# Performance work log

Hardware: AMD Instinct MI355X
Metric: run time of the kernel (lower is better)

## Reference

```python
import jax, jax.numpy as jnp
import numpy as np

DIM = 256
HEADS = 8
HEAD_DIM = DIM // HEADS
FFN = 1024
DIST_DECAY = 10.0
SCALING = HEAD_DIM ** -0.5
EPS = 1e-5


def _layer_norm(x, g, b):
    mu = jnp.mean(x, axis=-1, keepdims=True)
    var = jnp.mean((x - mu) ** 2, axis=-1, keepdims=True)
    return (x - mu) * jax.lax.rsqrt(var + EPS) * g + b


def setup_inputs() -> dict:
    key = jax.random.key(0)
    ks = jax.random.split(key, 20)
    B, N = 2, 192
    p = lambda k, shape: (jax.random.normal(k, shape, dtype=jnp.float32) * 0.02)
    return {
        "x": jax.random.normal(ks[0], (B, N, DIM), dtype=jnp.float32),
        "pos": jax.random.normal(ks[1], (B, N, 3), dtype=jnp.float32),
        "mask": jax.random.randint(ks[2], (B, N), 0, 2).astype(bool),
        "Wqkv": p(ks[3], (DIM, 3 * DIM)), "bqkv": jnp.zeros((3 * DIM,), jnp.float32),
        "W1": p(ks[4], (1, 4 * DIM)), "b1": jnp.zeros((4 * DIM,), jnp.float32),
        "W2": p(ks[5], (4 * DIM, DIM)), "b2": jnp.zeros((DIM,), jnp.float32),
        "Wo": p(ks[6], (DIM, DIM)), "bo": jnp.zeros((DIM,), jnp.float32),
        "ln1_g": jnp.ones((DIM,), jnp.float32), "ln1_b": jnp.zeros((DIM,), jnp.float32),
        "Wf1": p(ks[7], (DIM, FFN)), "bf1": jnp.zeros((FFN,), jnp.float32),
        "Wf2": p(ks[8], (FFN, DIM)), "bf2": jnp.zeros((DIM,), jnp.float32),
        "ln2_g": jnp.ones((DIM,), jnp.float32), "ln2_b": jnp.zeros((DIM,), jnp.float32),
    }


def _attention(x, pos, mask, Wqkv, bqkv, W1, b1, W2, b2, Wo, bo):
    B, N, _ = x.shape
    qkv = x @ Wqkv + bqkv
    q, k, v = jnp.split(qkv, 3, axis=-1)  # each [B,N,dim]
    diff = pos[:, :, None, :] - pos[:, None, :, :]          # [B,N,N,3]
    sq = jnp.sum(diff * diff, axis=-1, keepdims=True)        # [B,N,N,1]
    # safe sqrt (dist is 0 on diagonal)
    dist = jnp.sqrt(jnp.where(sq > 0, sq, 1.0)) * (sq > 0)
    de = jax.nn.relu(dist @ W1 + b1) @ W2 + b2               # [B,N,N,dim]
    decay = jnp.exp(-sq / DIST_DECAY)                        # [B,N,N,1]
    # w[b,i,j] = decay_ij * (k_i + de_ij) * q_j * scale
    w = decay * ((k[:, :, None, :] + de) * q[:, None, :, :] * SCALING)
    w = w.reshape(B, N, N, HEADS, HEAD_DIM)
    pm = mask[:, :, None] & mask[:, None, :]                 # [B,N,N]
    w = jnp.where(pm[..., None, None], -jnp.inf, w)
    w = jax.nn.softmax(w, axis=2)                            # per-channel softmax over j
    out = jnp.sum(v.reshape(B, 1, N, HEADS, HEAD_DIM) * w, axis=2)
    out = out.reshape(B, N, DIM)
    return out @ Wo + bo


def reference(x, pos, mask, Wqkv, bqkv, W1, b1, W2, b2, Wo, bo,
              ln1_g, ln1_b, Wf1, bf1, Wf2, bf2, ln2_g, ln2_b):
    # post-norm (encoder_normalize_before=False), dropout=0 (eval)
    res = x
    a = _attention(x, pos, mask, Wqkv, bqkv, W1, b1, W2, b2, Wo, bo)
    x = _layer_norm(res + a, ln1_g, ln1_b)
    res = x
    h = jax.nn.relu(x @ Wf1 + bf1) @ Wf2 + bf2
    x = _layer_norm(res + h, ln2_g, ln2_b)
    return x
```

## Files before the change

kernel.cpp:

```cpp
#include <hip/hip_runtime.h>
#include <math.h>

#define NB 2
#define NN 192
#define DIMX 256
#define HID 1024
#define NROWS (NB * NN)
#define SCALING 0.17677669529663687f
#define LOG2E 1.4426950408889634f
#define EPS 1e-5f

#define OFF_KK    0
#define OFF_QVP   (OFF_KK + NROWS * DIMX)
#define OFF_TSORT (OFF_QVP + NROWS * DIMX)
#define OFF_IDX   (OFF_TSORT + HID)
#define OFF_SCP   (OFF_IDX + HID)
#define OFF_ATT   (OFF_SCP + (HID + 1) * DIMX)
#define OFF_WB    (OFF_ATT + NROWS * DIMX)
#define WB_WO  0
#define WB_WF1 32768
#define WB_WF2 163840
#define WB_TOT 294912

typedef __fp16 half2_t __attribute__((ext_vector_type(2)));

__device__ inline unsigned int f2b(float f) {
  const unsigned int u = __float_as_uint(f);
  return (u + 0x7fffu + ((u >> 16) & 1u)) >> 16;
}
__device__ inline float blo(unsigned int u) {
  return __uint_as_float(u << 16);
}
__device__ inline float bhi(unsigned int u) {
  return __uint_as_float(u & 0xffff0000u);
}
__device__ inline unsigned int pkh(float a, float b) {
  union { half2_t h; unsigned int u; } x;
  x.h = __builtin_amdgcn_cvt_pkrtz(a, b);
  return x.u;
}
__device__ inline unsigned int pkh_rn(float a, float b) {
  union { half2_t h; unsigned int u; } x;
  x.h = half2_t{(__fp16)a, (__fp16)b};
  return x.u;
}
__device__ inline float fdot2u(unsigned int wu, unsigned int au, float c) {
  union { unsigned int u; half2_t h; } w, a;
  w.u = wu;
  a.u = au;
  return __builtin_amdgcn_fdot2(a.h, w.h, c, false);
}

__global__ __launch_bounds__(1024) void prep_kernel(
    const float* __restrict__ x, const float* __restrict__ Wqkv,
    const float* __restrict__ bqkv, const float* __restrict__ W1,
    const float* __restrict__ b1, const float* __restrict__ Wo,
    const float* __restrict__ Wf1, const float* __restrict__ Wf2,
    float* __restrict__ kk, unsigned int* __restrict__ qvp,
    float* __restrict__ t_sorted, int* __restrict__ idx_sorted,
    unsigned int* __restrict__ wb) {
  __shared__ float xs[4][DIMX];
  __shared__ float red[4][4][768];
  __shared__ float ts[HID];
  __shared__ int part[64][17];
  const int tid = threadIdx.x;
  const int bx = blockIdx.x;
  if (bx < 96) {
    const int r0 = bx * 4;
    const int kc = tid >> 8;
    const int c = tid & 255;
    xs[tid >> 8][tid & 255] = x[(r0 + (tid >> 8)) * DIMX + (tid & 255)];
    __syncthreads();
    float acc[4][3];
#pragma unroll
    for (int rr = 0; rr < 4; ++rr)
      for (int u = 0; u < 3; ++u) acc[rr][u] = 0.f;
    const int k0 = kc * 64;
#pragma unroll 4
    for (int i = 0; i < 64; ++i) {
      const int k = k0 + i;
      const float w0 = Wqkv[k * 768 + c];
      const float w1 = Wqkv[k * 768 + 256 + c];
      const float w2 = Wqkv[k * 768 + 512 + c];
#pragma unroll
      for (int rr = 0; rr < 4; ++rr) {
        const float xv = xs[rr][k];
        acc[rr][0] += xv * w0;
        acc[rr][1] += xv * w1;
        acc[rr][2] += xv * w2;
      }
    }
#pragma unroll
    for (int rr = 0; rr < 4; ++rr) {
      red[kc][rr][c] = acc[rr][0];
      red[kc][rr][256 + c] = acc[rr][1];
      red[kc][rr][512 + c] = acc[rr][2];
    }
    __syncthreads();
    {
      const int rr = tid >> 8;
      const int row = r0 + rr;
      const float q = red[0][rr][c] + red[1][rr][c] + red[2][rr][c] +
                      red[3][rr][c] + bqkv[c];
      const float kkv = red[0][rr][256 + c] + red[1][rr][256 + c] +
                        red[2][rr][256 + c] + red[3][rr][256 + c] +
                        bqkv[256 + c];
      const float v = red[0][rr][512 + c] + red[1][rr][512 + c] +
                      red[2][rr][512 + c] + red[3][rr][512 + c] +
                      bqkv[512 + c];
      kk[row * DIMX + c] = kkv;
      qvp[row * DIMX + c] = f2b(q * (SCALING * LOG2E)) | (f2b(v) << 16);
    }
  } else if (bx < 112) {
    const int bk = bx - 96;
    {
      const float w = W1[tid];
      ts[tid] = (w != 0.f) ? (-b1[tid] / w) : INFINITY;
    }
    __syncthreads();
    const int hl = tid >> 4;
    const int ck = tid & 15;
    const int h = bk * 64 + hl;
    const float t = ts[h];
    int cnt = 0;
    const int r0 = ck * 64;
#pragma unroll 4
    for (int rr = 0; rr < 64; ++rr) {
      const int r = r0 + rr;
      const float tv = ts[r];
      cnt += ((tv < t) || (tv == t && r < h)) ? 1 : 0;
    }
    part[hl][ck] = cnt;
    __syncthreads();
    if (ck == 0) {
      int rank = 0;
#pragma unroll
      for (int u = 0; u < 16; ++u) rank += part[hl][u];
      t_sorted[rank] = t;
      idx_sorted[rank] = h;
    }
  } else {
    const int p = (bx - 112) * 1024 + tid;
    if (p < WB_TOT) {
      float a, b;
      if (p < WB_WF1) {
        const int kp = p >> 8, cc = p & 255;
        a = Wo[(2 * kp) * DIMX + cc];
        b = Wo[(2 * kp + 1) * DIMX + cc];
      } else if (p < WB_WF2) {
        const int q = p - WB_WF1;
        const int kp = q >> 10, hh = q & 1023;
        a = Wf1[(2 * kp) * HID + hh];
        b = Wf1[(2 * kp + 1) * HID + hh];
      } else {
        const int q = p - WB_WF2;
        const int kp = q >> 8, cc = q & 255;
        a = Wf2[(2 * kp) * DIMX + cc];
        b = Wf2[(2 * kp + 1) * DIMX + cc];
      }
      wb[p] = pkh_rn(a, b);
    }
  }
}

__global__ __launch_bounds__(1024) void scan_kernel(
    const float* __restrict__ W1, const float* __restrict__ b1,
    const float* __restrict__ W2, const float* __restrict__ b2,
    const int* __restrict__ idx_sorted, unsigned int* __restrict__ SCp) {
  const int c = blockIdx.x;
  const int tid = threadIdx.x;
  const int lane = tid & 63;
  const int wid = tid >> 6;
  __shared__ float sW1[HID];
  __shared__ float sb1[HID];
  __shared__ int sidx[HID];
  __shared__ float bws[16], bwc[16], tws[16], twc[16];

  const float w = W1[tid];
  const float b1s = b1[tid];
  sW1[tid] = w;
  sb1[tid] = b1s;
  sidx[tid] = idx_sorted[tid];

  float bs = 0.f, bc = 0.f;
  {
    const float w2v = W2[tid * DIMX + c];
    if (w < 0.f) {
      bs = w * w2v;
      bc = b1s * w2v;
    } else if (w == 0.f && b1s > 0.f) {
      bc = b1s * w2v;
    }
  }
  for (int off = 32; off > 0; off >>= 1) {
    bs += __shfl_down(bs, off);
    bc += __shfl_down(bc, off);
  }
  __syncthreads();

  float vS, vC;
  {
    const int hh = sidx[tid];
    const float w1v = sW1[hh];
    const float sign = (w1v > 0.f) ? 1.f : -1.f;
    const float coefS = (w1v == 0.f) ? 0.f : sign * w1v;
    const float coefC = (w1v == 0.f) ? 0.f : sign * sb1[hh];
    const float w2v = W2[hh * DIMX + c];
    vS = coefS * w2v;
    vC = coefC * w2v;
  }
  for (int off = 1; off < 64; off <<= 1) {
    const float tS_ = __shfl_up(vS, off);
    const float tC_ = __shfl_up(vC, off);
    if (lane >= off) {
      vS += tS_;
      vC += tC_;
    }
  }
  if (lane == 0) {
    bws[wid] = bs;
    bwc[wid] = bc;
  }
  if (lane == 63) {
    tws[wid] = vS;
    twc[wid] = vC;
  }
  __syncthreads();
  float S0 = 0.f, C0 = 0.f, offS = 0.f, offC = 0.f;
#pragma unroll
  for (int u = 0; u < 16; ++u) {
    S0 += bws[u];
    C0 += bwc[u];
    if (u < wid) {
      offS += tws[u];
      offC += twc[u];
    }
  }
  C0 += b2[c];
  SCp[(tid + 1) * DIMX + c] = f2b(S0 + offS + vS) | (f2b(C0 + offC + vC) << 16);
  if (tid == 0) SCp[c] = f2b(S0) | (f2b(C0) << 16);
}

__global__ __launch_bounds__(1024) void attn_kernel(
    const float* __restrict__ pos, const int* __restrict__ mask,
    const float* __restrict__ kk, const unsigned int* __restrict__ qvp,
    const float* __restrict__ t_sorted, const unsigned int* __restrict__ SCp,
    float* __restrict__ att) {
  __shared__ float tS[HID];
  __shared__ float posB[NN][3];
  __shared__ int maskB[NN];
  __shared__ float dJ[NN];
  __shared__ float decJ[NN];
  __shared__ int segJ[NN];
  __shared__ int pmJ[NN];
  __shared__ float sl[4][DIMX];
  __shared__ float so[4][DIMX];

  const int r = blockIdx.x;
  const int b = r / NN;
  const int i = r % NN;
  const int tid = threadIdx.x;
  const int c = tid & 255;
  const int jq = tid >> 8;

  tS[tid] = t_sorted[tid];
  if (tid < NN) {
    posB[tid][0] = pos[(b * NN + tid) * 3 + 0];
    posB[tid][1] = pos[(b * NN + tid) * 3 + 1];
    posB[tid][2] = pos[(b * NN + tid) * 3 + 2];
    maskB[tid] = mask[b * NN + tid];
  }
  __syncthreads();

  if (tid < NN) {
    const int j = tid;
    const float dx = posB[j][0] - posB[i][0];
    const float dy = posB[j][1] - posB[i][1];
    const float dz = posB[j][2] - posB[i][2];
    const float sq = dx * dx + dy * dy + dz * dz;
    const float d = (sq > 0.f) ? sqrtf(sq) : 0.f;
    dJ[j] = d;
    decJ[j] = __expf(-sq * 0.1f);
    int lo = 0, hi = HID;
    while (lo < hi) {
      const int mid = (lo + hi) >> 1;
      if (tS[mid] <= d) lo = mid + 1;
      else hi = mid;
    }
    segJ[j] = lo;
    pmJ[j] = maskB[i] && maskB[j];
  }
  __syncthreads();

  const float kc_ = kk[(b * NN + i) * DIMX + c];
  float l = 0.f, o = 0.f;
  const int j0 = jq * 48;
#pragma unroll 4
  for (int jj = 0; jj < 48; ++jj) {
    const int j = j0 + jj;
    const int seg = segJ[j];
    const unsigned int scu = SCp[seg * DIMX + c];
    const float de = fmaf(dJ[j], blo(scu), bhi(scu));
    const unsigned int qvu = qvp[(b * NN + j) * DIMX + c];
    const float sval = decJ[j] * blo(qvu) * (kc_ + de);
    const float p = pmJ[j] ? 0.f : exp2f(sval);
    l += p;
    o = fmaf(p, bhi(qvu), o);
  }
  sl[jq][c] = l;
  so[jq][c] = o;
  __syncthreads();
  if (tid < DIMX) {
    const float lt = sl[0][tid] + sl[1][tid] + sl[2][tid] + sl[3][tid];
    const float ot = so[0][tid] + so[1][tid] + so[2][tid] + so[3][tid];
    att[r * DIMX + tid] = ot / lt;
  }
}

__global__ __launch_bounds__(1024) void tail_kernel(
    const float* __restrict__ att, const float* __restrict__ x,
    const unsigned int* __restrict__ woH, const float* __restrict__ bo,
    const float* __restrict__ ln1g, const float* __restrict__ ln1b,
    const uint4* __restrict__ wf1H, const float* __restrict__ bf1,
    const uint4* __restrict__ wf2H, const float* __restrict__ bf2,
    const float* __restrict__ ln2g, const float* __restrict__ ln2b,
    float* __restrict__ out) {
  __shared__ float4 red[16][2][64];
  __shared__ unsigned int attsH[2][128];
  __shared__ unsigned int x1sH[2][128];
  __shared__ unsigned int hidsH[2][512];
  __shared__ float x1tmp[2][DIMX];
  __shared__ float hidtmp[2][HID];
  __shared__ float lr1[8], lr2[8];
  const int r0 = blockIdx.x * 2;
  const int tid = threadIdx.x;
  const int rr = tid >> 8;
  const int c = tid & 255;

  if (tid < 256) {
    const int rr2 = tid >> 7, c2 = tid & 127;
    const float2 f = ((const float2*)att)[(r0 + rr2) * 128 + c2];
    attsH[rr2][c2] = pkh(f.x, f.y);
  }
  __syncthreads();

  {
    const int ks = tid >> 8;
    float a0 = 0.f, a1 = 0.f;
#pragma unroll 8
    for (int i = 0; i < 32; ++i) {
      const int kp = ks * 32 + i;
      const unsigned int wu = woH[kp * 256 + c];
      a0 = fdot2u(wu, attsH[0][kp], a0);
      a1 = fdot2u(wu, attsH[1][kp], a1);
    }
    float* redp = (float*)red;
    redp[(ks * 2 + 0) * 256 + c] = a0;
    redp[(ks * 2 + 1) * 256 + c] = a1;
  }
  __syncthreads();
  float t1 = 0.f, x1v = 0.f;
  if (rr < 2) {
    const float* redp = (const float*)red;
    const float pv = redp[(0 * 2 + rr) * 256 + c] + redp[(1 * 2 + rr) * 256 + c] +
                     redp[(2 * 2 + rr) * 256 + c] + redp[(3 * 2 + rr) * 256 + c];
    t1 = pv + x[(r0 + rr) * DIMX + c] + bo[c];
  }
  {
    float s1 = t1, s2 = t1 * t1;
    for (int off = 32; off > 0; off >>= 1) {
      s1 += __shfl_down(s1, off);
      s2 += __shfl_down(s2, off);
    }
    if ((tid & 63) == 0 && tid < 512) { lr1[tid >> 6] = s1; lr2[tid >> 6] = s2; }
  }
  __syncthreads();
  if (rr < 2) {
    const int base = rr * 4;
    const float S1 = lr1[base] + lr1[base + 1] + lr1[base + 2] + lr1[base + 3];
    const float S2 = lr2[base] + lr2[base + 1] + lr2[base + 2] + lr2[base + 3];
    const float mu = S1 * (1.f / DIMX);
    const float var = S2 * (1.f / DIMX) - mu * mu;
    x1v = (t1 - mu) * rsqrtf(var + EPS) * ln1g[c] + ln1b[c];
    x1tmp[rr][c] = x1v;
  }
  __syncthreads();
  if (tid < 256) {
    const int rr2 = tid >> 7, c2 = tid & 127;
    x1sH[rr2][c2] = pkh(x1tmp[rr2][2 * c2], x1tmp[rr2][2 * c2 + 1]);
  }
  __syncthreads();

  {
    const int ks = tid >> 8, h4 = tid & 255;
    float4 a0 = {0.f, 0.f, 0.f, 0.f}, a1 = {0.f, 0.f, 0.f, 0.f};
#pragma unroll 4
    for (int i = 0; i < 32; ++i) {
      const int kp = ks * 32 + i;
      const uint4 wv = wf1H[kp * 256 + h4];
      const unsigned int xa = x1sH[0][kp], xb = x1sH[1][kp];
      a0.x = fdot2u(wv.x, xa, a0.x);
      a0.y = fdot2u(wv.y, xa, a0.y);
      a0.z = fdot2u(wv.z, xa, a0.z);
      a0.w = fdot2u(wv.w, xa, a0.w);
      a1.x = fdot2u(wv.x, xb, a1.x);
      a1.y = fdot2u(wv.y, xb, a1.y);
      a1.z = fdot2u(wv.z, xb, a1.z);
      a1.w = fdot2u(wv.w, xb, a1.w);
    }
    float4* redf4 = (float4*)red;
    redf4[(ks * 2 + 0) * 256 + h4] = a0;
    redf4[(ks * 2 + 1) * 256 + h4] = a1;
  }
  __syncthreads();
  {
    const float* redf = (const float*)red;
    const float bf = bf1[tid];
    const float v0 = redf[0 * 1024 + tid] + redf[2 * 1024 + tid] +
                     redf[4 * 1024 + tid] + redf[6 * 1024 + tid];
    const float v1 = redf[1 * 1024 + tid] + redf[3 * 1024 + tid] +
                     redf[5 * 1024 + tid] + redf[7 * 1024 + tid];
    hidtmp[0][tid] = fmaxf(v0 + bf, 0.f);
    hidtmp[1][tid] = fmaxf(v1 + bf, 0.f);
  }
  __syncthreads();
  {
    const int rr2 = tid >> 9, c2 = tid & 511;
    hidsH[rr2][c2] = pkh(hidtmp[rr2][2 * c2], hidtmp[rr2][2 * c2 + 1]);
  }
  __syncthreads();

  {
    const int ks = tid >> 6, c4 = tid & 63;
    float4 a0 = {0.f, 0.f, 0.f, 0.f}, a1 = {0.f, 0.f, 0.f, 0.f};
#pragma unroll 4
    for (int i = 0; i < 32; ++i) {
      const int kp = ks * 32 + i;
      const uint4 wv = wf2H[kp * 64 + c4];
      const unsigned int ha = hidsH[0][kp], hb = hidsH[1][kp];
      a0.x = fdot2u(wv.x, ha, a0.x);
      a0.y = fdot2u(wv.y, ha, a0.y);
      a0.z = fdot2u(wv.z, ha, a0.z);
      a0.w = fdot2u(wv.w, ha, a0.w);
      a1.x = fdot2u(wv.x, hb, a1.x);
      a1.y = fdot2u(wv.y, hb, a1.y);
      a1.z = fdot2u(wv.z, hb, a1.z);
      a1.w = fdot2u(wv.w, hb, a1.w);
    }
    red[ks][0][c4] = a0;
    red[ks][1][c4] = a1;
  }
  __syncthreads();
  float t2 = 0.f;
  if (rr < 2) {
    const int c4 = c >> 2, cm = c & 3;
    float pv = 0.f;
#pragma unroll
    for (int u = 0; u < 16; ++u) pv += ((const float*)&red[u][rr][c4])[cm];
    t2 = pv + x1v + bf2[c];
  }
  {
    float s1 = t2, s2 = t2 * t2;
    for (int off = 32; off > 0; off >>= 1) {
      s1 += __shfl_down(s1, off);
      s2 += __shfl_down(s2, off);
    }
    if ((tid & 63) == 0 && tid < 512) { lr1[tid >> 6] = s1; lr2[tid >> 6] = s2; }
  }
  __syncthreads();
  if (rr < 2) {
    const int base = rr * 4;
    const float S1 = lr1[base] + lr1[base + 1] + lr1[base + 2] + lr1[base + 3];
    const float S2 = lr2[base] + lr2[base + 1] + lr2[base + 2] + lr2[base + 3];
    const float mu = S1 * (1.f / DIMX);
    const float var = S2 * (1.f / DIMX) - mu * mu;
    out[(r0 + rr) * DIMX + c] = (t2 - mu) * rsqrtf(var + EPS) * ln2g[c] + ln2b[c];
  }
}

extern "C" void kernel_launch(void* const* d_in, const int* in_sizes, int n_in,
                              void* d_out, int out_size, void* d_ws,
                              size_t ws_size, hipStream_t stream) {
  const float* x = (const float*)d_in[0];
  const float* pos = (const float*)d_in[1];
  const int* mask = (const int*)d_in[2];
  const float* Wqkv = (const float*)d_in[3];
  const float* bqkv = (const float*)d_in[4];
  const float* W1 = (const float*)d_in[5];
  const float* b1 = (const float*)d_in[6];
  const float* W2 = (const float*)d_in[7];
  const float* b2 = (const float*)d_in[8];
  const float* Wo = (const float*)d_in[9];
  const float* bo = (const float*)d_in[10];
  const float* ln1g = (const float*)d_in[11];
  const float* ln1b = (const float*)d_in[12];
  const float* Wf1 = (const float*)d_in[13];
  const float* bf1 = (const float*)d_in[14];
  const float* Wf2 = (const float*)d_in[15];
  const float* bf2 = (const float*)d_in[16];
  const float* ln2g = (const float*)d_in[17];
  const float* ln2b = (const float*)d_in[18];

  float* ws = (float*)d_ws;
  float* kk = ws + OFF_KK;
  unsigned int* qvp = (unsigned int*)(ws + OFF_QVP);
  float* t_sorted = ws + OFF_TSORT;
  int* idx_sorted = (int*)(ws + OFF_IDX);
  unsigned int* SCp = (unsigned int*)(ws + OFF_SCP);
  float* att = ws + OFF_ATT;
  unsigned int* wb = (unsigned int*)(ws + OFF_WB);
  float* outp = (float*)d_out;

  hipLaunchKernelGGL(prep_kernel, dim3(400), dim3(1024), 0, stream, x, Wqkv,
                     bqkv, W1, b1, Wo, Wf1, Wf2, kk, qvp, t_sorted, idx_sorted,
                     wb);
  hipLaunchKernelGGL(scan_kernel, dim3(DIMX), dim3(1024), 0, stream, W1, b1,
                     W2, b2, idx_sorted, SCp);
  hipLaunchKernelGGL(attn_kernel, dim3(NROWS), dim3(1024), 0, stream, pos,
                     mask, kk, qvp, t_sorted, SCp, att);
  hipLaunchKernelGGL(tail_kernel, dim3(NROWS / 2), dim3(1024), 0, stream, att,
                     x, (const unsigned int*)(wb + WB_WO), bo, ln1g, ln1b,
                     (const uint4*)(wb + WB_WF1), bf1,
                     (const uint4*)(wb + WB_WF2), bf2, ln2g, ln2b, outp);
}
```

Measured before the change: 57.98 us.

## Move QKV projection into scan kernel using packed fp16 weights and fdot2

The sort and fp16 weight packing now run in the first kernel, which also packs Wqkv into fp16 pairs. The QKV projection moves into the second kernel next to the 256 scan blocks, and it reads half-size packed weights and x through fdot2. The aim is to balance work across the two early launches and halve the Wqkv bandwidth. In exchange, the QKV projection is computed in fp16, and it now waits on the weight conversion in the first kernel.

```diff
diff --git a/kernel.cpp b/kernel.cpp
--- a/kernel.cpp
+++ b/kernel.cpp
@@ -17,10 +17,11 @@
 #define OFF_SCP   (OFF_IDX + HID)
 #define OFF_ATT   (OFF_SCP + (HID + 1) * DIMX)
 #define OFF_WB    (OFF_ATT + NROWS * DIMX)
-#define WB_WO  0
-#define WB_WF1 32768
-#define WB_WF2 163840
-#define WB_TOT 294912
+#define WB_QKVH 0
+#define WB_WO   98304
+#define WB_WF1  131072
+#define WB_WF2  262144
+#define WB_TOT  393216
 
 typedef __fp16 half2_t __attribute__((ext_vector_type(2)));
 
@@ -51,43 +52,112 @@
   return __builtin_amdgcn_fdot2(a.h, w.h, c, false);
 }
 
-__global__ __launch_bounds__(1024) void prep_kernel(
-    const float* __restrict__ x, const float* __restrict__ Wqkv,
-    const float* __restrict__ bqkv, const float* __restrict__ W1,
-    const float* __restrict__ b1, const float* __restrict__ Wo,
+__global__ __launch_bounds__(1024) void sortconv_kernel(
+    const float* __restrict__ W1, const float* __restrict__ b1,
+    const float* __restrict__ Wqkv, const float* __restrict__ Wo,
     const float* __restrict__ Wf1, const float* __restrict__ Wf2,
-    float* __restrict__ kk, unsigned int* __restrict__ qvp,
     float* __restrict__ t_sorted, int* __restrict__ idx_sorted,
     unsigned int* __restrict__ wb) {
-  __shared__ float xs[4][DIMX];
-  __shared__ float red[4][4][768];
   __shared__ float ts[HID];
   __shared__ int part[64][17];
+  const int tid = threadIdx.x;
+  const int bx = blockIdx.x;
+  if (bx < 16) {
+    {
+      const float w = W1[tid];
+      ts[tid] = (w != 0.f) ? (-b1[tid] / w) : INFINITY;
+    }
+    __syncthreads();
+    const int hl = tid >> 4;
+    const int ck = tid & 15;
+    const int h = bx * 64 + hl;
+    const float t = ts[h];
+    int cnt = 0;
+    const int r0 = ck * 64;
+#pragma unroll 4
+    for (int rr = 0; rr < 64; ++rr) {
+      const int r = r0 + rr;
+      const float tv = ts[r];
+      cnt += ((tv < t) || (tv == t && r < h)) ? 1 : 0;
+    }
+    part[hl][ck] = cnt;
+    __syncthreads();
+    if (ck == 0) {
+      int rank = 0;
+#pragma unroll
+      for (int u = 0; u < 16; ++u) rank += part[hl][u];
+      t_sorted[rank] = t;
+      idx_sorted[rank] = h;
+    }
+  } else {
+    const int p = (bx - 16) * 1024 + tid;
+    float a, b;
+    if (p < WB_WO) {
+      const int kp = p / 768, col = p % 768;
+      a = Wqkv[(2 * kp) * 768 + col];
+      b = Wqkv[(2 * kp + 1) * 768 + col];
+    } else if (p < WB_WF1) {
+      const int q = p - WB_WO;
+      const int kp = q >> 8, cc = q & 255;
+      a = Wo[(2 * kp) * DIMX + cc];
+      b = Wo[(2 * kp + 1) * DIMX + cc];
+    } else if (p < WB_WF2) {
+      const int q = p - WB_WF1;
+      const int kp = q >> 10, hh = q & 1023;
+      a = Wf1[(2 * kp) * HID + hh];
+      b = Wf1[(2 * kp + 1) * HID + hh];
+    } else {
+      const int q = p - WB_WF2;
+      const int kp = q >> 8, cc = q & 255;
+      a = Wf2[(2 * kp) * DIMX + cc];
+      b = Wf2[(2 * kp + 1) * DIMX + cc];
+    }
+    wb[p] = pkh_rn(a, b);
+  }
+}
+
+__global__ __launch_bounds__(1024) void qkvscan_kernel(
+    const float* __restrict__ x, const unsigned int* __restrict__ wqkvH,
+    const float* __restrict__ bqkv, const float* __restrict__ W1,
+    const float* __restrict__ b1, const float* __restrict__ W2,
+    const float* __restrict__ b2, const int* __restrict__ idx_sorted,
+    float* __restrict__ kk, unsigned int* __restrict__ qvp,
+    unsigned int* __restrict__ SCp) {
+  __shared__ unsigned int xsH[4][128];
+  __shared__ float red[4][4][768];
+  __shared__ float sW1[HID];
+  __shared__ float sb1[HID];
+  __shared__ int sidx[HID];
+  __shared__ float bws[16], bwc[16], tws[16], twc[16];
   const int tid = threadIdx.x;
   const int bx = blockIdx.x;
   if (bx < 96) {
     const int r0 = bx * 4;
     const int kc = tid >> 8;
     const int c = tid & 255;
-    xs[tid >> 8][tid & 255] = x[(r0 + (tid >> 8)) * DIMX + (tid & 255)];
+    if (tid < 512) {
+      const int rr2 = tid >> 7, c2 = tid & 127;
+      const float2 f = ((const float2*)x)[(r0 + rr2) * 128 + c2];
+      xsH[rr2][c2] = pkh(f.x, f.y);
+    }
     __syncthreads();
     float acc[4][3];
 #pragma unroll
     for (int rr = 0; rr < 4; ++rr)
       for (int u = 0; u < 3; ++u) acc[rr][u] = 0.f;
-    const int k0 = kc * 64;
+    const int kp0 = kc * 32;
 #pragma unroll 4
-    for (int i = 0; i < 64; ++i) {
-      const int k = k0 + i;
-      const float w0 = Wqkv[k * 768 + c];
-      const float w1 = Wqkv[k * 768 + 256 + c];
-      const float w2 = Wqkv[k * 768 + 512 + c];
+    for (int i = 0; i < 32; ++i) {
+      const int kp = kp0 + i;
+      const unsigned int w0 = wqkvH[kp * 768 + c];
+      const unsigned int w1 = wqkvH[kp * 768 + 256 + c];
+      const unsigned int w2 = wqkvH[kp * 768 + 512 + c];
 #pragma unroll
       for (int rr = 0; rr < 4; ++rr) {
-        const float xv = xs[rr][k];
-        acc[rr][0] += xv * w0;
-        acc[rr][1] += xv * w1;
-        acc[rr][2] += xv * w2;
+        const unsigned int xa = xsH[rr][kp];
+        acc[rr][0] = fdot2u(w0, xa, acc[rr][0]);
+        acc[rr][1] = fdot2u(w1, xa, acc[rr][1]);
+        acc[rr][2] = fdot2u(w2, xa, acc[rr][2]);
       }
     }
 #pragma unroll
@@ -111,134 +181,75 @@
       kk[row * DIMX + c] = kkv;
       qvp[row * DIMX + c] = f2b(q * (SCALING * LOG2E)) | (f2b(v) << 16);
     }
-  } else if (bx < 112) {
-    const int bk = bx - 96;
+  } else {
+    const int c = bx - 96;
+    const int lane = tid & 63;
+    const int wid = tid >> 6;
+
+    const float w = W1[tid];
+    const float b1s = b1[tid];
+    sW1[tid] = w;
+    sb1[tid] = b1s;
+    sidx[tid] = idx_sorted[tid];
+
+    float bs = 0.f, bc = 0.f;
     {
-      const float w = W1[tid];
-      ts[tid] = (w != 0.f) ? (-b1[tid] / w) : INFINITY;
+      const float w2v = W2[tid * DIMX + c];
+      if (w < 0.f) {
+        bs = w * w2v;
+        bc = b1s * w2v;
+      } else if (w == 0.f && b1s > 0.f) {
+        bc = b1s * w2v;
+      }
+    }
+    for (int off = 32; off > 0; off >>= 1) {
+      bs += __shfl_down(bs, off);
+      bc += __shfl_down(bc, off);
     }
     __syncthreads();
-    const int hl = tid >> 4;
-    const int ck = tid & 15;
-    const int h = bk * 64 + hl;
-    const float t = ts[h];
-    int cnt = 0;
-    const int r0 = ck * 64;
-#pragma unroll 4
-    for (int rr = 0; rr < 64; ++rr) {
-      const int r = r0 + rr;
-      const float tv = ts[r];
-      cnt += ((tv < t) || (tv == t && r < h)) ? 1 : 0;
-    }
-    part[hl][ck] = cnt;
+
+    float vS, vC;
+    {
+      const int hh = sidx[tid];
+      const float w1v = sW1[hh];
+      const float sign = (w1v > 0.f) ? 1.f : -1.f;
+      const float coefS = (w1v == 0.f) ? 0.f : sign * w1v;
+      const float coefC = (w1v == 0.f) ? 0.f : sign * sb1[hh];
+      const float w2v = W2[hh * DIMX + c];
+      vS = coefS * w2v;
+      vC = coefC * w2v;
+    }
+    for (int off = 1; off < 64; off <<= 1) {
+      const float tS_ = __shfl_up(vS, off);
+      const float tC_ = __shfl_up(vC, off);
+      if (lane >= off) {
+        vS += tS_;
+        vC += tC_;
+      }
+    }
+    if (lane == 0) {
+      bws[wid] = bs;
+      bwc[wid] = bc;
+    }
+    if (lane == 63) {
+      tws[wid] = vS;
+      twc[wid] = vC;
+    }
     __syncthreads();
-    if (ck == 0) {
-      int rank = 0;
+    float S0 = 0.f, C0 = 0.f, offS = 0.f, offC = 0.f;
 #pragma unroll
-      for (int u = 0; u < 16; ++u) rank += part[hl][u];
-      t_sorted[rank] = t;
-      idx_sorted[rank] = h;
-    }
-  } else {
-    const int p = (bx - 112) * 1024 + tid;
-    if (p < WB_TOT) {
-      float a, b;
-      if (p < WB_WF1) {
-        const int kp = p >> 8, cc = p & 255;
-        a = Wo[(2 * kp) * DIMX + cc];
-        b = Wo[(2 * kp + 1) * DIMX + cc];
-      } else if (p < WB_WF2) {
-        const int q = p - WB_WF1;
-        const int kp = q >> 10, hh = q & 1023;
-        a = Wf1[(2 * kp) * HID + hh];
-        b = Wf1[(2 * kp + 1) * HID + hh];
-      } else {
-        const int q = p - WB_WF2;
-        const int kp = q >> 8, cc = q & 255;
-        a = Wf2[(2 * kp) * DIMX + cc];
-        b = Wf2[(2 * kp + 1) * DIMX + cc];
+    for (int u = 0; u < 16; ++u) {
+      S0 += bws[u];
+      C0 += bwc[u];
+      if (u < wid) {
+        offS += tws[u];
+        offC += twc[u];
       }
-      wb[p] = pkh_rn(a, b);
-    }
-  }
-}
-
-__global__ __launch_bounds__(1024) void scan_kernel(
-    const float* __restrict__ W1, const float* __restrict__ b1,
-    const float* __restrict__ W2, const float* __restrict__ b2,
-    const int* __restrict__ idx_sorted, unsigned int* __restrict__ SCp) {
-  const int c = blockIdx.x;
-  const int tid = threadIdx.x;
-  const int lane = tid & 63;
-  const int wid = tid >> 6;
-  __shared__ float sW1[HID];
-  __shared__ float sb1[HID];
-  __shared__ int sidx[HID];
-  __shared__ float bws[16], bwc[16], tws[16], twc[16];
-
-  const float w = W1[tid];
-  const float b1s = b1[tid];
-  sW1[tid] = w;
-  sb1[tid] = b1s;
-  sidx[tid] = idx_sorted[tid];
-
-  float bs = 0.f, bc = 0.f;
-  {
-    const float w2v = W2[tid * DIMX + c];
-    if (w < 0.f) {
-      bs = w * w2v;
-      bc = b1s * w2v;
-    } else if (w == 0.f && b1s > 0.f) {
-      bc = b1s * w2v;
-    }
-  }
-  for (int off = 32; off > 0; off >>= 1) {
-    bs += __shfl_down(bs, off);
-    bc += __shfl_down(bc, off);
-  }
-  __syncthreads();
-
-  float vS, vC;
-  {
-    const int hh = sidx[tid];
-    const float w1v = sW1[hh];
-    const float sign = (w1v > 0.f) ? 1.f : -1.f;
-    const float coefS = (w1v == 0.f) ? 0.f : sign * w1v;
-    const float coefC = (w1v == 0.f) ? 0.f : sign * sb1[hh];
-    const float w2v = W2[hh * DIMX + c];
-    vS = coefS * w2v;
-    vC = coefC * w2v;
-  }
-  for (int off = 1; off < 64; off <<= 1) {
-    const float tS_ = __shfl_up(vS, off);
-    const float tC_ = __shfl_up(vC, off);
-    if (lane >= off) {
-      vS += tS_;
-      vC += tC_;
-    }
-  }
-  if (lane == 0) {
-    bws[wid] = bs;
-    bwc[wid] = bc;
-  }
-  if (lane == 63) {
-    tws[wid] = vS;
-    twc[wid] = vC;
-  }
-  __syncthreads();
-  float S0 = 0.f, C0 = 0.f, offS = 0.f, offC = 0.f;
-#pragma unroll
-  for (int u = 0; u < 16; ++u) {
-    S0 += bws[u];
-    C0 += bwc[u];
-    if (u < wid) {
-      offS += tws[u];
-      offC += twc[u];
-    }
-  }
-  C0 += b2[c];
-  SCp[(tid + 1) * DIMX + c] = f2b(S0 + offS + vS) | (f2b(C0 + offC + vC) << 16);
-  if (tid == 0) SCp[c] = f2b(S0) | (f2b(C0) << 16);
+    }
+    C0 += b2[c];
+    SCp[(tid + 1) * DIMX + c] = f2b(S0 + offS + vS) | (f2b(C0 + offC + vC) << 16);
+    if (tid == 0) SCp[c] = f2b(S0) | (f2b(C0) << 16);
+  }
 }
 
 __global__ __launch_bounds__(1024) void attn_kernel(
@@ -511,15 +522,15 @@
   unsigned int* wb = (unsigned int*)(ws + OFF_WB);
   float* outp = (float*)d_out;
 
-  hipLaunchKernelGGL(prep_kernel, dim3(400), dim3(1024), 0, stream, x, Wqkv,
-                     bqkv, W1, b1, Wo, Wf1, Wf2, kk, qvp, t_sorted, idx_sorted,
-                     wb);
-  hipLaunchKernelGGL(scan_kernel, dim3(DIMX), dim3(1024), 0, stream, W1, b1,
-                     W2, b2, idx_sorted, SCp);
+  hipLaunchKernelGGL(sortconv_kernel, dim3(400), dim3(1024), 0, stream, W1,
+                     b1, Wqkv, Wo, Wf1, Wf2, t_sorted, idx_sorted, wb);
+  hipLaunchKernelGGL(qkvscan_kernel, dim3(352), dim3(1024), 0, stream, x,
+                     wb + WB_QKVH, bqkv, W1, b1, W2, b2, idx_sorted, kk, qvp,
+                     SCp);
   hipLaunchKernelGGL(attn_kernel, dim3(NROWS), dim3(1024), 0, stream, pos,
                      mask, kk, qvp, t_sorted, SCp, att);
   hipLaunchKernelGGL(tail_kernel, dim3(NROWS / 2), dim3(1024), 0, stream, att,
-                     x, (const unsigned int*)(wb + WB_WO), bo, ln1g, ln1b,
+                     x, wb + WB_WO, bo, ln1g, ln1b,
                      (const uint4*)(wb + WB_WF1), bf1,
                      (const uint4*)(wb + WB_WF2), bf2, ln2g, ln2b, outp);
 }
```

New measurement: 61.90 us. 1.07x slower.
